# Kernel tuning notes

Hardware: AMD Instinct MI355X
Metric: run time of the kernel (lower is better)

Reference implementation:

```python
import jax, jax.numpy as jnp
import numpy as np


def _gcn_conv(x, src, dst, norm, W, b, n_nodes):
    # x: [N, Fin] -> [N, Fout]. PyG GCNConv: linear (no bias), normalized
    # scatter-add aggregation over edges (self-loops already in src/dst), + bias.
    h = x @ W                                  # [N, Fout]
    msg = h[src] * norm[:, None]               # [E+N, Fout]
    out = jax.ops.segment_sum(msg, dst, num_segments=n_nodes)
    return out + b


def _prep_edges(edge_index, n_nodes):
    # Add self-loops and compute symmetric normalization deg^-1/2 * deg^-1/2.
    loops = jnp.arange(n_nodes, dtype=edge_index.dtype)
    src = jnp.concatenate([edge_index[0], loops])
    dst = jnp.concatenate([edge_index[1], loops])
    deg = jax.ops.segment_sum(jnp.ones_like(dst, dtype=jnp.float32), dst,
                              num_segments=n_nodes)
    dinv = jnp.where(deg > 0, jax.lax.rsqrt(jnp.maximum(deg, 1.0)), 0.0)
    norm = dinv[src] * dinv[dst]
    return src, dst, norm


def setup_inputs() -> dict:
    key = jax.random.key(0)
    k1, k2, k3, k4 = jax.random.split(key, 4)
    N, Fin, Fout = 50000, 128, 64
    H = 2 * Fout
    E = 640000
    x = jax.random.normal(k1, (N, Fin), dtype=jnp.float32)
    edge_index = jax.random.randint(k2, (2, E), 0, N, dtype=jnp.int64)
    W1 = jax.random.normal(k3, (Fin, H), dtype=jnp.float32) * (1.0 / np.sqrt(Fin))
    b1 = jnp.zeros((H,), dtype=jnp.float32)
    W2 = jax.random.normal(k4, (H, Fout), dtype=jnp.float32) * (1.0 / np.sqrt(H))
    b2 = jnp.zeros((Fout,), dtype=jnp.float32)
    return {"x": x, "edge_index": edge_index, "W1": W1, "b1": b1, "W2": W2, "b2": b2}


def reference(x, edge_index, W1, b1, W2, b2):
    n_nodes = x.shape[0]
    src, dst, norm = _prep_edges(edge_index, n_nodes)
    h = _gcn_conv(x, src, dst, norm, W1, b1, n_nodes)
    h = jax.nn.relu(h)
    return _gcn_conv(h, src, dst, norm, W2, b2, n_nodes)
```

## Files before the change

kernel.cpp:

```cpp
#include <hip/hip_runtime.h>

#define CEILDIV(a,b) (((a)+(b)-1)/(b))

constexpr int CAP = 64;


__device__ __forceinline__ unsigned short f2bf(float f) {
  union { float f; unsigned u; } v; v.f = f;
  unsigned u = v.u + (0x7fffu + ((v.u >> 16) & 1u));
  return (unsigned short)(u >> 16);
}
__device__ __forceinline__ unsigned pack2(float lo, float hi) {
  return (unsigned)f2bf(lo) | ((unsigned)f2bf(hi) << 16);
}
__device__ __forceinline__ void add2(float* a, unsigned w) {
  union { unsigned u; float f; } lo, hi;
  lo.u = w << 16; hi.u = w & 0xffff0000u;
  a[0] += lo.f; a[1] += hi.f;
}
__device__ __forceinline__ void add8(float* a, uint4 w) {
  add2(a + 0, w.x); add2(a + 2, w.y); add2(a + 4, w.z); add2(a + 6, w.w);
}
__device__ __forceinline__ void fma2(float* a, unsigned w, float s) {
  union { unsigned u; float f; } lo, hi;
  lo.u = w << 16; hi.u = w & 0xffff0000u;
  a[0] = fmaf(lo.f, s, a[0]); a[1] = fmaf(hi.f, s, a[1]);
}
__device__ __forceinline__ void fma8(float* a, uint4 w, float s) {
  fma2(a + 0, w.x, s); fma2(a + 2, w.y, s); fma2(a + 4, w.z, s); fma2(a + 6, w.w, s);
}


__global__ __launch_bounds__(256) void k_init(const int* __restrict__ raw,
                                              int* __restrict__ flag,
                                              int* __restrict__ cnt, int N, int E) {
  const int tid = threadIdx.x;
  const int i4 = (blockIdx.x * 256 + tid) * 4;
  if (i4 + 3 < N) {
    *(int4*)&cnt[i4] = make_int4(0, 0, 0, 0);
  } else {
    for (int j = 0; j < 4; ++j)
      if (i4 + j < N) cnt[i4 + j] = 0;
  }
  if (blockIdx.x == 0) {
    __shared__ int ok;
    if (tid == 0) ok = 1;
    __syncthreads();
    int n = (E < 1024) ? E : 1024;
    for (int i = tid; i < n; i += 256)
      if (raw[2 * i + 1] != 0) ok = 0;
    __syncthreads();
    if (tid == 0) *flag = ok;
  }
}

template <int K, int NO, bool XBF16, bool SCALE>
__device__ __forceinline__ void gemm_body(const void* __restrict__ Xv,
                                          const float* __restrict__ W,
                                          const int* __restrict__ cnt,
                                          unsigned short* __restrict__ Y,
                                          int N, int bid) {
  constexpr int ROWS = 128, KC = 64, TC = NO / 16;
  constexpr int XST = ROWS + 4;
  constexpr int WST = NO + 4;
  __shared__ float xs[KC * XST];
  __shared__ float ws[KC * WST];
  const int tid = threadIdx.x;
  const int tx = tid & 15, ty = tid >> 4;
  const int c0 = tx * TC, r0 = ty * 8;
  const int row0 = bid * ROWS;

  float acc[8][TC];
#pragma unroll
  for (int i = 0; i < 8; ++i)
#pragma unroll
    for (int j = 0; j < TC; ++j) acc[i][j] = 0.0f;

  for (int kk = 0; kk < K; kk += KC) {
#pragma unroll
    for (int it = 0; it < (ROWS * KC / 4) / 256; ++it) {
      int idx = it * 256 + tid;
      int r = idx >> 4, kq = idx & 15;
      int row = row0 + r; if (row >= N) row = N - 1;
      float f0, f1, f2, f3;
      if constexpr (XBF16) {
        const unsigned short* Xb = (const unsigned short*)Xv;
        uint2 v = *(const uint2*)&Xb[(size_t)row * K + kk + kq * 4];
        union { unsigned u; float f; } t0, t1, t2, t3;
        t0.u = v.x << 16; t1.u = v.x & 0xffff0000u;
        t2.u = v.y << 16; t3.u = v.y & 0xffff0000u;
        f0 = t0.f; f1 = t1.f; f2 = t2.f; f3 = t3.f;
      } else {
        const float* Xf = (const float*)Xv;
        float4 v = *(const float4*)&Xf[(size_t)row * K + kk + kq * 4];
        f0 = v.x; f1 = v.y; f2 = v.z; f3 = v.w;
      }
      xs[(kq * 4 + 0) * XST + r] = f0;
      xs[(kq * 4 + 1) * XST + r] = f1;
      xs[(kq * 4 + 2) * XST + r] = f2;
      xs[(kq * 4 + 3) * XST + r] = f3;
    }
#pragma unroll
    for (int it = 0; it < (KC * NO / 4) / 256; ++it) {
      int idx = it * 256 + tid;
      int c4 = idx & (NO / 4 - 1), kw = idx / (NO / 4);
      float4 v = *(const float4*)&W[(size_t)(kk + kw) * NO + c4 * 4];
      *(float4*)&ws[kw * WST + c4 * 4] = v;
    }
    __syncthreads();
#pragma unroll 4
    for (int k = 0; k < KC; ++k) {
      const float4 xa = *(const float4*)&xs[k * XST + r0];
      const float4 xb = *(const float4*)&xs[k * XST + r0 + 4];
      float4 wv[TC / 4];
#pragma unroll
      for (int j4 = 0; j4 < TC / 4; ++j4)
        wv[j4] = *(const float4*)&ws[k * WST + c0 + j4 * 4];
      const float xr[8] = {xa.x, xa.y, xa.z, xa.w, xb.x, xb.y, xb.z, xb.w};
#pragma unroll
      for (int i = 0; i < 8; ++i)
#pragma unroll
        for (int j4 = 0; j4 < TC / 4; ++j4) {
          acc[i][j4 * 4 + 0] += xr[i] * wv[j4].x;
          acc[i][j4 * 4 + 1] += xr[i] * wv[j4].y;
          acc[i][j4 * 4 + 2] += xr[i] * wv[j4].z;
          acc[i][j4 * 4 + 3] += xr[i] * wv[j4].w;
        }
    }
    __syncthreads();
  }
#pragma unroll
  for (int i = 0; i < 8; ++i) {
    int r = row0 + r0 + i;
    if (r < N) {
      float dv = SCALE ? rsqrtf((float)(cnt[r] + 1)) : 1.0f;
      unsigned pk[TC / 2];
#pragma unroll
      for (int j = 0; j < TC / 2; ++j)
        pk[j] = pack2(acc[i][2 * j] * dv, acc[i][2 * j + 1] * dv);
      if constexpr (TC == 8) {
        *(uint4*)&Y[(size_t)r * NO + c0] = make_uint4(pk[0], pk[1], pk[2], pk[3]);
      } else {
        *(uint2*)&Y[(size_t)r * NO + c0] = make_uint2(pk[0], pk[1]);
      }
    }
  }
}

__global__ __launch_bounds__(256, 2) void k_fused(
    const float* __restrict__ X, const float* __restrict__ W1,
    unsigned short* __restrict__ hb1, int N, int GB,
    const int* __restrict__ raw, const int* __restrict__ flag,
    int* __restrict__ cnt, int* __restrict__ esrc, int E, int FB) {
  const int i = blockIdx.x;
  const int m = (FB < GB) ? FB : GB;
  int fid = -1, gid = -1;
  if (i < 2 * m) {
    if ((i & 1) == 0) fid = i >> 1; else gid = i >> 1;
  } else {
    int r = i - 2 * m;
    if (FB > GB) fid = m + r; else gid = m + r;
  }

  if (gid >= 0) {
    gemm_body<128, 128, false, false>(X, W1, nullptr, hb1, N, gid);
    return;
  }

  int e0 = (fid * 256 + threadIdx.x) * 4;
  if (e0 >= E) return;
  const bool is64 = (*flag != 0);
  if (((E & 3) == 0) && e0 + 3 < E) {
    int s[4], d[4];
    if (is64) {
      uint4 sa = *(const uint4*)&raw[2 * e0];
      uint4 sb = *(const uint4*)&raw[2 * e0 + 4];
      uint4 da = *(const uint4*)&raw[2 * (E + e0)];
      uint4 db = *(const uint4*)&raw[2 * (E + e0) + 4];
      s[0] = (int)sa.x; s[1] = (int)sa.z; s[2] = (int)sb.x; s[3] = (int)sb.z;
      d[0] = (int)da.x; d[1] = (int)da.z; d[2] = (int)db.x; d[3] = (int)db.z;
    } else {
      uint4 sv = *(const uint4*)&raw[e0];
      uint4 dv = *(const uint4*)&raw[E + e0];
      s[0] = (int)sv.x; s[1] = (int)sv.y; s[2] = (int)sv.z; s[3] = (int)sv.w;
      d[0] = (int)dv.x; d[1] = (int)dv.y; d[2] = (int)dv.z; d[3] = (int)dv.w;
    }
    int p[4];
#pragma unroll
    for (int j = 0; j < 4; ++j) p[j] = atomicAdd(&cnt[d[j]], 1);
#pragma unroll
    for (int j = 0; j < 4; ++j)
      if (p[j] < CAP) esrc[(size_t)d[j] * CAP + p[j]] = s[j];
  } else {
    for (int e = e0; e < E && e < e0 + 4; ++e) {
      int s = is64 ? raw[2 * e] : raw[e];
      int d = is64 ? raw[2 * (E + e)] : raw[E + e];
      int pos = atomicAdd(&cnt[d], 1);
      if (pos < CAP) esrc[(size_t)d * CAP + pos] = s;
    }
  }
}

__global__ __launch_bounds__(256) void k_agg1(const unsigned short* __restrict__ h,
                                              const int* __restrict__ cnt,
                                              const int* __restrict__ esrc,
                                              const float* __restrict__ bias,
                                              unsigned short* __restrict__ out,
                                              int N) {
  const int v = blockIdx.x * 16 + (threadIdx.x >> 4);
  if (v >= N) return;
  const int lc = threadIdx.x & 15;
  const uint4* __restrict__ h4 = (const uint4*)h;

  const int cv = cnt[v];
  const int deg = min(cv, CAP);
  const float dv = rsqrtf((float)(cv + 1));
  float acc[8] = {0, 0, 0, 0, 0, 0, 0, 0};
  fma8(acc, h4[(size_t)v * 16 + lc], dv);
  const int* __restrict__ ep = &esrc[(size_t)v * CAP];
  int e = 0;
  for (; e + 4 <= deg; e += 4) {
    int s0 = ep[e + 0], s1 = ep[e + 1], s2 = ep[e + 2], s3 = ep[e + 3];
    float w0 = rsqrtf((float)(cnt[s0] + 1));
    float w1 = rsqrtf((float)(cnt[s1] + 1));
    float w2 = rsqrtf((float)(cnt[s2] + 1));
    float w3 = rsqrtf((float)(cnt[s3] + 1));
    uint4 a0 = h4[(size_t)s0 * 16 + lc];
    uint4 a1 = h4[(size_t)s1 * 16 + lc];
    uint4 a2 = h4[(size_t)s2 * 16 + lc];
    uint4 a3 = h4[(size_t)s3 * 16 + lc];
    fma8(acc, a0, w0); fma8(acc, a1, w1); fma8(acc, a2, w2); fma8(acc, a3, w3);
  }
  for (; e < deg; ++e) {
    int s = ep[e];
    fma8(acc, h4[(size_t)s * 16 + lc], rsqrtf((float)(cnt[s] + 1)));
  }

  const float4 b0 = *(const float4*)&bias[lc * 8];
  const float4 b1 = *(const float4*)&bias[lc * 8 + 4];
  float r[8];
  r[0] = fmaxf(acc[0] * dv + b0.x, 0.0f);
  r[1] = fmaxf(acc[1] * dv + b0.y, 0.0f);
  r[2] = fmaxf(acc[2] * dv + b0.z, 0.0f);
  r[3] = fmaxf(acc[3] * dv + b0.w, 0.0f);
  r[4] = fmaxf(acc[4] * dv + b1.x, 0.0f);
  r[5] = fmaxf(acc[5] * dv + b1.y, 0.0f);
  r[6] = fmaxf(acc[6] * dv + b1.z, 0.0f);
  r[7] = fmaxf(acc[7] * dv + b1.w, 0.0f);
  uint4 pk = make_uint4(pack2(r[0], r[1]), pack2(r[2], r[3]),
                        pack2(r[4], r[5]), pack2(r[6], r[7]));
  ((uint4*)out)[(size_t)v * 16 + lc] = pk;
}

__global__ __launch_bounds__(256, 2) void k_gemm2(const unsigned short* __restrict__ X,
                                                  const float* __restrict__ W,
                                                  const int* __restrict__ cnt,
                                                  unsigned short* __restrict__ Y,
                                                  int N) {
  gemm_body<128, 64, true, true>(X, W, cnt, Y, N, blockIdx.x);
}

template <int F>
__global__ __launch_bounds__(256) void k_agg2(const unsigned short* __restrict__ h,
                                              const int* __restrict__ cnt,
                                              const int* __restrict__ esrc,
                                              const float* __restrict__ bias,
                                              float* __restrict__ out, int N) {
  constexpr int LPN = F / 8;
  constexpr int NPB = 256 / LPN;
  const int v = blockIdx.x * NPB + threadIdx.x / LPN;
  if (v >= N) return;
  const int lc = threadIdx.x % LPN;
  const uint4* __restrict__ h4 = (const uint4*)h;

  float acc[8] = {0, 0, 0, 0, 0, 0, 0, 0};
  add8(acc, h4[(size_t)v * LPN + lc]);
  const int cv = cnt[v];
  const int deg = min(cv, CAP);
  const float dv = rsqrtf((float)(cv + 1));
  const int* __restrict__ ep = &esrc[(size_t)v * CAP];
  int e = 0;
  for (; e + 4 <= deg; e += 4) {
    int s0 = ep[e + 0], s1 = ep[e + 1], s2 = ep[e + 2], s3 = ep[e + 3];
    uint4 a0 = h4[(size_t)s0 * LPN + lc];
    uint4 a1 = h4[(size_t)s1 * LPN + lc];
    uint4 a2 = h4[(size_t)s2 * LPN + lc];
    uint4 a3 = h4[(size_t)s3 * LPN + lc];
    add8(acc, a0); add8(acc, a1); add8(acc, a2); add8(acc, a3);
  }
  for (; e < deg; ++e) add8(acc, h4[(size_t)ep[e] * LPN + lc]);

  const float4 b0 = *(const float4*)&bias[lc * 8];
  const float4 b1 = *(const float4*)&bias[lc * 8 + 4];
  float4 o0, o1;
  o0.x = acc[0] * dv + b0.x; o0.y = acc[1] * dv + b0.y;
  o0.z = acc[2] * dv + b0.z; o0.w = acc[3] * dv + b0.w;
  o1.x = acc[4] * dv + b1.x; o1.y = acc[5] * dv + b1.y;
  o1.z = acc[6] * dv + b1.z; o1.w = acc[7] * dv + b1.w;
  float4* op = (float4*)(out + (size_t)v * F + lc * 8);
  op[0] = o0; op[1] = o1;
}


extern "C" void kernel_launch(void* const* d_in, const int* in_sizes, int n_in,
                              void* d_out, int out_size, void* d_ws, size_t ws_size,
                              hipStream_t stream) {
  const float* x  = (const float*)d_in[0];
  const int*   ei = (const int*)d_in[1];
  const float* W1 = (const float*)d_in[2];
  const float* b1 = (const float*)d_in[3];
  const float* W2 = (const float*)d_in[4];
  const float* b2 = (const float*)d_in[5];
  const int H    = in_sizes[3];
  const int Fin  = in_sizes[2] / H;
  const int N    = in_sizes[0] / Fin;
  const int E    = in_sizes[1] / 2;
  const int FO   = in_sizes[5];
  float* outp = (float*)d_out;

  char* p = (char*)d_ws;
  auto alloc = [&](size_t bytes) {
    void* q = (void*)p;
    p += (bytes + 255) & ~(size_t)255;
    return q;
  };
  int*   flag = (int*)alloc(256);
  int*   cnt  = (int*)alloc((size_t)N * 4);
  int*   esrc = (int*)alloc((size_t)N * CAP * 4);
  unsigned short* hb1 = (unsigned short*)alloc((size_t)N * H * 2);
  unsigned short* ab1 = (unsigned short*)alloc((size_t)N * H * 2);
  unsigned short* hb2 = (unsigned short*)alloc((size_t)N * FO * 2);

  const int NB = CEILDIV(N, 1024);
  const int FB = CEILDIV(E, 1024);
  const int GB = CEILDIV(N, 128);

  k_init<<<NB, 256, 0, stream>>>(ei, flag, cnt, N, E);
  k_fused<<<FB + GB, 256, 0, stream>>>(x, W1, hb1, N, GB, ei, flag, cnt, esrc, E, FB);
  k_agg1<<<CEILDIV(N, 16), 256, 0, stream>>>(hb1, cnt, esrc, b1, ab1, N);
  k_gemm2<<<CEILDIV(N, 128), 256, 0, stream>>>(ab1, W2, cnt, hb2, N);
  k_agg2<64><<<CEILDIV(N, 32), 256, 0, stream>>>(hb2, cnt, esrc, b2, outp, N);
}
```

Baseline: 129.6 us.

## Split fused fill/GEMM1, prescale GEMM1 output by source degree, swizzle shared memory

Splits the combined edge-bucketing and first GEMM kernel into two separate launches. The first GEMM can then scale each output row by its source-degree factor, which removes the per-edge rsqrt and count gather from the first aggregation, now a plain bf16 sum. It also XOR-swizzles the X tile in shared memory and interleaves W column reads to cut LDS bank conflicts, and changes each thread's output columns to two 4-wide strips. The cost is losing the overlap between the atomic edge fill and GEMM1, plus one extra kernel launch.

```diff
diff --git a/kernel.cpp b/kernel.cpp
--- a/kernel.cpp
+++ b/kernel.cpp
@@ -20,14 +20,6 @@
 }
 __device__ __forceinline__ void add8(float* a, uint4 w) {
   add2(a + 0, w.x); add2(a + 2, w.y); add2(a + 4, w.z); add2(a + 6, w.w);
-}
-__device__ __forceinline__ void fma2(float* a, unsigned w, float s) {
-  union { unsigned u; float f; } lo, hi;
-  lo.u = w << 16; hi.u = w & 0xffff0000u;
-  a[0] = fmaf(lo.f, s, a[0]); a[1] = fmaf(hi.f, s, a[1]);
-}
-__device__ __forceinline__ void fma8(float* a, uint4 w, float s) {
-  fma2(a + 0, w.x, s); fma2(a + 2, w.y, s); fma2(a + 4, w.z, s); fma2(a + 6, w.w, s);
 }
 
 
@@ -54,7 +46,43 @@
   }
 }
 
-template <int K, int NO, bool XBF16, bool SCALE>
+__global__ void k_fill(const int* __restrict__ raw, const int* __restrict__ flag,
+                       int* __restrict__ cnt, int* __restrict__ esrc, int E) {
+  int e0 = (blockIdx.x * blockDim.x + threadIdx.x) * 4;
+  if (e0 >= E) return;
+  const bool is64 = (*flag != 0);
+  if (((E & 3) == 0) && e0 + 3 < E) {
+    int s[4], d[4];
+    if (is64) {
+      uint4 sa = *(const uint4*)&raw[2 * e0];
+      uint4 sb = *(const uint4*)&raw[2 * e0 + 4];
+      uint4 da = *(const uint4*)&raw[2 * (E + e0)];
+      uint4 db = *(const uint4*)&raw[2 * (E + e0) + 4];
+      s[0] = (int)sa.x; s[1] = (int)sa.z; s[2] = (int)sb.x; s[3] = (int)sb.z;
+      d[0] = (int)da.x; d[1] = (int)da.z; d[2] = (int)db.x; d[3] = (int)db.z;
+    } else {
+      uint4 sv = *(const uint4*)&raw[e0];
+      uint4 dv = *(const uint4*)&raw[E + e0];
+      s[0] = (int)sv.x; s[1] = (int)sv.y; s[2] = (int)sv.z; s[3] = (int)sv.w;
+      d[0] = (int)dv.x; d[1] = (int)dv.y; d[2] = (int)dv.z; d[3] = (int)dv.w;
+    }
+    int p[4];
+#pragma unroll
+    for (int j = 0; j < 4; ++j) p[j] = atomicAdd(&cnt[d[j]], 1);
+#pragma unroll
+    for (int j = 0; j < 4; ++j)
+      if (p[j] < CAP) esrc[(size_t)d[j] * CAP + p[j]] = s[j];
+  } else {
+    for (int e = e0; e < E && e < e0 + 4; ++e) {
+      int s = is64 ? raw[2 * e] : raw[e];
+      int d = is64 ? raw[2 * (E + e)] : raw[E + e];
+      int pos = atomicAdd(&cnt[d], 1);
+      if (pos < CAP) esrc[(size_t)d * CAP + pos] = s;
+    }
+  }
+}
+
+template <int K, int NO, bool XBF16>
 __device__ __forceinline__ void gemm_body(const void* __restrict__ Xv,
                                           const float* __restrict__ W,
                                           const int* __restrict__ cnt,
@@ -67,7 +95,7 @@
   __shared__ float ws[KC * WST];
   const int tid = threadIdx.x;
   const int tx = tid & 15, ty = tid >> 4;
-  const int c0 = tx * TC, r0 = ty * 8;
+  const int r0 = ty * 8;
   const int row0 = bid * ROWS;
 
   float acc[8][TC];
@@ -95,10 +123,11 @@
         float4 v = *(const float4*)&Xf[(size_t)row * K + kk + kq * 4];
         f0 = v.x; f1 = v.y; f2 = v.z; f3 = v.w;
       }
-      xs[(kq * 4 + 0) * XST + r] = f0;
-      xs[(kq * 4 + 1) * XST + r] = f1;
-      xs[(kq * 4 + 2) * XST + r] = f2;
-      xs[(kq * 4 + 3) * XST + r] = f3;
+      const int rs = r ^ ((kq & 7) << 2);
+      xs[(kq * 4 + 0) * XST + rs] = f0;
+      xs[(kq * 4 + 1) * XST + rs] = f1;
+      xs[(kq * 4 + 2) * XST + rs] = f2;
+      xs[(kq * 4 + 3) * XST + rs] = f3;
     }
 #pragma unroll
     for (int it = 0; it < (KC * NO / 4) / 256; ++it) {
@@ -110,12 +139,14 @@
     __syncthreads();
 #pragma unroll 4
     for (int k = 0; k < KC; ++k) {
-      const float4 xa = *(const float4*)&xs[k * XST + r0];
-      const float4 xb = *(const float4*)&xs[k * XST + r0 + 4];
+      const int Xk = ((k >> 2) & 7) << 2;
+      const int xbase = k * XST + (r0 ^ (Xk & 24));
+      const float4 xa = *(const float4*)&xs[xbase + (Xk & 4)];
+      const float4 xb = *(const float4*)&xs[xbase + ((Xk & 4) ^ 4)];
       float4 wv[TC / 4];
-#pragma unroll
-      for (int j4 = 0; j4 < TC / 4; ++j4)
-        wv[j4] = *(const float4*)&ws[k * WST + c0 + j4 * 4];
+      wv[0] = *(const float4*)&ws[k * WST + tx * 4];
+      if constexpr (TC == 8)
+        wv[1] = *(const float4*)&ws[k * WST + 64 + tx * 4];
       const float xr[8] = {xa.x, xa.y, xa.z, xa.w, xb.x, xb.y, xb.z, xb.w};
 #pragma unroll
       for (int i = 0; i < 8; ++i)
@@ -133,72 +164,33 @@
   for (int i = 0; i < 8; ++i) {
     int r = row0 + r0 + i;
     if (r < N) {
-      float dv = SCALE ? rsqrtf((float)(cnt[r] + 1)) : 1.0f;
-      unsigned pk[TC / 2];
-#pragma unroll
-      for (int j = 0; j < TC / 2; ++j)
-        pk[j] = pack2(acc[i][2 * j] * dv, acc[i][2 * j + 1] * dv);
+      const float dv = rsqrtf((float)(cnt[r] + 1));
+      uint2 pa = make_uint2(pack2(acc[i][0] * dv, acc[i][1] * dv),
+                            pack2(acc[i][2] * dv, acc[i][3] * dv));
+      *(uint2*)&Y[(size_t)r * NO + tx * 4] = pa;
       if constexpr (TC == 8) {
-        *(uint4*)&Y[(size_t)r * NO + c0] = make_uint4(pk[0], pk[1], pk[2], pk[3]);
-      } else {
-        *(uint2*)&Y[(size_t)r * NO + c0] = make_uint2(pk[0], pk[1]);
+        uint2 pb = make_uint2(pack2(acc[i][4] * dv, acc[i][5] * dv),
+                              pack2(acc[i][6] * dv, acc[i][7] * dv));
+        *(uint2*)&Y[(size_t)r * NO + 64 + tx * 4] = pb;
       }
     }
   }
 }
 
-__global__ __launch_bounds__(256, 2) void k_fused(
-    const float* __restrict__ X, const float* __restrict__ W1,
-    unsigned short* __restrict__ hb1, int N, int GB,
-    const int* __restrict__ raw, const int* __restrict__ flag,
-    int* __restrict__ cnt, int* __restrict__ esrc, int E, int FB) {
-  const int i = blockIdx.x;
-  const int m = (FB < GB) ? FB : GB;
-  int fid = -1, gid = -1;
-  if (i < 2 * m) {
-    if ((i & 1) == 0) fid = i >> 1; else gid = i >> 1;
-  } else {
-    int r = i - 2 * m;
-    if (FB > GB) fid = m + r; else gid = m + r;
-  }
-
-  if (gid >= 0) {
-    gemm_body<128, 128, false, false>(X, W1, nullptr, hb1, N, gid);
-    return;
-  }
-
-  int e0 = (fid * 256 + threadIdx.x) * 4;
-  if (e0 >= E) return;
-  const bool is64 = (*flag != 0);
-  if (((E & 3) == 0) && e0 + 3 < E) {
-    int s[4], d[4];
-    if (is64) {
-      uint4 sa = *(const uint4*)&raw[2 * e0];
-      uint4 sb = *(const uint4*)&raw[2 * e0 + 4];
-      uint4 da = *(const uint4*)&raw[2 * (E + e0)];
-      uint4 db = *(const uint4*)&raw[2 * (E + e0) + 4];
-      s[0] = (int)sa.x; s[1] = (int)sa.z; s[2] = (int)sb.x; s[3] = (int)sb.z;
-      d[0] = (int)da.x; d[1] = (int)da.z; d[2] = (int)db.x; d[3] = (int)db.z;
-    } else {
-      uint4 sv = *(const uint4*)&raw[e0];
-      uint4 dv = *(const uint4*)&raw[E + e0];
-      s[0] = (int)sv.x; s[1] = (int)sv.y; s[2] = (int)sv.z; s[3] = (int)sv.w;
-      d[0] = (int)dv.x; d[1] = (int)dv.y; d[2] = (int)dv.z; d[3] = (int)dv.w;
-    }
-    int p[4];
-#pragma unroll
-    for (int j = 0; j < 4; ++j) p[j] = atomicAdd(&cnt[d[j]], 1);
-#pragma unroll
-    for (int j = 0; j < 4; ++j)
-      if (p[j] < CAP) esrc[(size_t)d[j] * CAP + p[j]] = s[j];
-  } else {
-    for (int e = e0; e < E && e < e0 + 4; ++e) {
-      int s = is64 ? raw[2 * e] : raw[e];
-      int d = is64 ? raw[2 * (E + e)] : raw[E + e];
-      int pos = atomicAdd(&cnt[d], 1);
-      if (pos < CAP) esrc[(size_t)d * CAP + pos] = s;
-    }
-  }
+__global__ __launch_bounds__(256, 2) void k_gemm1(const float* __restrict__ X,
+                                                  const float* __restrict__ W,
+                                                  const int* __restrict__ cnt,
+                                                  unsigned short* __restrict__ Y,
+                                                  int N) {
+  gemm_body<128, 128, false>(X, W, cnt, Y, N, blockIdx.x);
+}
+
+__global__ __launch_bounds__(256, 2) void k_gemm2(const unsigned short* __restrict__ X,
+                                                  const float* __restrict__ W,
+                                                  const int* __restrict__ cnt,
+                                                  unsigned short* __restrict__ Y,
+                                                  int N) {
+  gemm_body<128, 64, true>(X, W, cnt, Y, N, blockIdx.x);
 }
 
 __global__ __launch_bounds__(256) void k_agg1(const unsigned short* __restrict__ h,
@@ -212,29 +204,22 @@
   const int lc = threadIdx.x & 15;
   const uint4* __restrict__ h4 = (const uint4*)h;
 
+  float acc[8] = {0, 0, 0, 0, 0, 0, 0, 0};
+  add8(acc, h4[(size_t)v * 16 + lc]);
   const int cv = cnt[v];
   const int deg = min(cv, CAP);
   const float dv = rsqrtf((float)(cv + 1));
-  float acc[8] = {0, 0, 0, 0, 0, 0, 0, 0};
-  fma8(acc, h4[(size_t)v * 16 + lc], dv);
   const int* __restrict__ ep = &esrc[(size_t)v * CAP];
   int e = 0;
   for (; e + 4 <= deg; e += 4) {
     int s0 = ep[e + 0], s1 = ep[e + 1], s2 = ep[e + 2], s3 = ep[e + 3];
-    float w0 = rsqrtf((float)(cnt[s0] + 1));
-    float w1 = rsqrtf((float)(cnt[s1] + 1));
-    float w2 = rsqrtf((float)(cnt[s2] + 1));
-    float w3 = rsqrtf((float)(cnt[s3] + 1));
     uint4 a0 = h4[(size_t)s0 * 16 + lc];
     uint4 a1 = h4[(size_t)s1 * 16 + lc];
     uint4 a2 = h4[(size_t)s2 * 16 + lc];
     uint4 a3 = h4[(size_t)s3 * 16 + lc];
-    fma8(acc, a0, w0); fma8(acc, a1, w1); fma8(acc, a2, w2); fma8(acc, a3, w3);
-  }
-  for (; e < deg; ++e) {
-    int s = ep[e];
-    fma8(acc, h4[(size_t)s * 16 + lc], rsqrtf((float)(cnt[s] + 1)));
-  }
+    add8(acc, a0); add8(acc, a1); add8(acc, a2); add8(acc, a3);
+  }
+  for (; e < deg; ++e) add8(acc, h4[(size_t)ep[e] * 16 + lc]);
 
   const float4 b0 = *(const float4*)&bias[lc * 8];
   const float4 b1 = *(const float4*)&bias[lc * 8 + 4];
@@ -252,22 +237,12 @@
   ((uint4*)out)[(size_t)v * 16 + lc] = pk;
 }
 
-__global__ __launch_bounds__(256, 2) void k_gemm2(const unsigned short* __restrict__ X,
-                                                  const float* __restrict__ W,
-                                                  const int* __restrict__ cnt,
-                                                  unsigned short* __restrict__ Y,
-                                                  int N) {
-  gemm_body<128, 64, true, true>(X, W, cnt, Y, N, blockIdx.x);
-}
-
-template <int F>
 __global__ __launch_bounds__(256) void k_agg2(const unsigned short* __restrict__ h,
                                               const int* __restrict__ cnt,
                                               const int* __restrict__ esrc,
                                               const float* __restrict__ bias,
                                               float* __restrict__ out, int N) {
-  constexpr int LPN = F / 8;
-  constexpr int NPB = 256 / LPN;
+  constexpr int F = 64, LPN = 8, NPB = 32;
   const int v = blockIdx.x * NPB + threadIdx.x / LPN;
   if (v >= N) return;
   const int lc = threadIdx.x % LPN;
@@ -332,12 +307,12 @@
   unsigned short* hb2 = (unsigned short*)alloc((size_t)N * FO * 2);
 
   const int NB = CEILDIV(N, 1024);
-  const int FB = CEILDIV(E, 1024);
-  const int GB = CEILDIV(N, 128);
-
   k_init<<<NB, 256, 0, stream>>>(ei, flag, cnt, N, E);
-  k_fused<<<FB + GB, 256, 0, stream>>>(x, W1, hb1, N, GB, ei, flag, cnt, esrc, E, FB);
+  k_fill<<<CEILDIV(E, 1024), 256, 0, stream>>>(ei, flag, cnt, esrc, E);
+
+  k_gemm1<<<CEILDIV(N, 128), 256, 0, stream>>>(x, W1, cnt, hb1, N);
   k_agg1<<<CEILDIV(N, 16), 256, 0, stream>>>(hb1, cnt, esrc, b1, ab1, N);
+
   k_gemm2<<<CEILDIV(N, 128), 256, 0, stream>>>(ab1, W2, cnt, hb2, N);
-  k_agg2<64><<<CEILDIV(N, 32), 256, 0, stream>>>(hb2, cnt, esrc, b2, outp, N);
-}
+  k_agg2<<<CEILDIV(N, 32), 256, 0, stream>>>(hb2, cnt, esrc, b2, outp, N);
+}
```

Result: slower. 136.8 us (+5.5%).
